# Optimization experiments

Measured on AMD Instinct MI355X. Metric: run time of the kernel, lower is better.

The kernel has to match this reference:

```python
import jax, jax.numpy as jnp
import numpy as np
from jax import lax

D = 1024      # d_model
NH = 16       # n_head
CA = 384      # adapter_channels
T = 16        # num_frames
B = 4         # videos
L = 257       # tokens = 16*16 patches + CLS
HW = 16       # spatial side


def setup_inputs() -> dict:
    key = jax.random.key(0)
    ks = jax.random.split(key, 12)
    s = 0.02
    f = lambda k, shp: jax.random.normal(k, shp, jnp.float32) * s
    return {
        'x': jax.random.normal(ks[0], (B * T, L, D), jnp.float32),
        'ln1_g': jnp.ones((D,), jnp.float32), 'ln1_b': jnp.zeros((D,), jnp.float32),
        'w_in': f(ks[1], (3 * D, D)), 'b_in': jnp.zeros((3 * D,), jnp.float32),
        'w_out': f(ks[2], (D, D)), 'b_out': jnp.zeros((D,), jnp.float32),
        'o_fc1_w': f(ks[3], (CA, D)), 'o_fc1_b': jnp.zeros((CA,), jnp.float32),
        'o_conv_w': f(ks[4], (3, 3, 1, CA)), 'o_conv_b': jnp.zeros((CA,), jnp.float32),
        'o_fc2_w': f(ks[5], (D, CA)), 'o_fc2_b': jnp.zeros((D,), jnp.float32),
        'a_fc1_w': f(ks[6], (CA, D)), 'a_fc1_b': jnp.zeros((CA,), jnp.float32),
        'a_conv_w': f(ks[7], (3, 1, CA)), 'a_conv_b': jnp.zeros((CA,), jnp.float32),
        'a_fc2_w': f(ks[8], (D, CA)), 'a_fc2_b': jnp.zeros((D,), jnp.float32),
        'ln2_g': jnp.ones((D,), jnp.float32), 'ln2_b': jnp.zeros((D,), jnp.float32),
        'mlp_fc_w': f(ks[9], (4 * D, D)), 'mlp_fc_b': jnp.zeros((4 * D,), jnp.float32),
        'mlp_proj_w': f(ks[10], (D, 4 * D)), 'mlp_proj_b': jnp.zeros((D,), jnp.float32),
    }


def _ln(x, g, b):
    # fp32 LayerNorm (matches CLIP LayerNorm subclass)
    x32 = x.astype(jnp.float32)
    mu = jnp.mean(x32, -1, keepdims=True)
    var = jnp.mean(jnp.square(x32 - mu), -1, keepdims=True)
    return ((x32 - mu) * lax.rsqrt(var + 1e-5) * g + b).astype(x.dtype)


def _mha(x, w_in, b_in, w_out, b_out):
    BT, Lq, C = x.shape
    hd = C // NH
    qkv = x @ w_in.T + b_in                       # (BT, L, 3C)
    q, k, v = jnp.split(qkv, 3, axis=-1)
    sh = lambda t: t.reshape(BT, Lq, NH, hd).transpose(0, 2, 1, 3)  # (BT, H, L, hd)
    q, k, v = sh(q), sh(k), sh(v)
    scores = jnp.einsum('bhqd,bhkd->bhqk', q * (hd ** -0.5), k)
    attn = jax.nn.softmax(scores, axis=-1)
    out = jnp.einsum('bhqk,bhkd->bhqd', attn, v)
    out = out.transpose(0, 2, 1, 3).reshape(BT, Lq, C)
    return out @ w_out.T + b_out


def _offset_adapter(x, fc1_w, fc1_b, conv_w, conv_b, fc2_w, fc2_b):
    BT, Lx, C = x.shape
    Bv = BT // T
    xs = x[:, 1:, :].reshape(Bv, T, Lx - 1, C)          # drop CLS
    former = jnp.concatenate([xs[:, :1], xs[:, :-1]], axis=1)
    off = xs - former                                    # temporal diff
    off = off @ fc1_w.T + fc1_b                          # (B, T, HW*HW, Ca)
    off = off.reshape(Bv * T, HW, HW, CA)
    # depthwise (1,3,3) Conv3d: kernel size 1 along T -> per-frame 3x3 depthwise conv
    off = lax.conv_general_dilated(off, conv_w, (1, 1), [(1, 1), (1, 1)],
                                   dimension_numbers=('NHWC', 'HWIO', 'NHWC'),
                                   feature_group_count=CA) + conv_b
    off = off.reshape(BT, Lx - 1, CA)
    return off @ fc2_w.T + fc2_b                         # (BT, L-1, C)


def _adapter2(x, a_fc1_w, a_fc1_b, a_conv_w, a_conv_b, a_fc2_w, a_fc2_b,
              o_fc1_w, o_fc1_b, o_conv_w, o_conv_b, o_fc2_w, o_fc2_b):
    BT, Lx, C = x.shape
    Bv = BT // T
    off = _offset_adapter(x, o_fc1_w, o_fc1_b, o_conv_w, o_conv_b, o_fc2_w, o_fc2_b)
    y = x @ a_fc1_w.T + a_fc1_b                          # (BT, L, Ca)
    y = y.reshape(Bv, T, Lx, CA).transpose(0, 2, 1, 3).reshape(Bv * Lx, T, CA)
    # depthwise Conv1d along the temporal axis
    y = lax.conv_general_dilated(y, a_conv_w, (1,), [(1, 1)],
                                 dimension_numbers=('NWC', 'WIO', 'NWC'),
                                 feature_group_count=CA) + a_conv_b
    y = y.reshape(Bv, Lx, T, CA).transpose(0, 2, 1, 3).reshape(BT, Lx, CA)
    y = y @ a_fc2_w.T + a_fc2_b                          # (BT, L, C)
    x_id = x.at[:, 1:, :].add(off)
    return y + x_id


def _block(x, ln1_g, ln1_b, w_in, b_in, w_out, b_out,
           a_fc1_w, a_fc1_b, a_conv_w, a_conv_b, a_fc2_w, a_fc2_b,
           o_fc1_w, o_fc1_b, o_conv_w, o_conv_b, o_fc2_w, o_fc2_b,
           ln2_g, ln2_b, mlp_fc_w, mlp_fc_b, mlp_proj_w, mlp_proj_b):
    x = x + _mha(_ln(x, ln1_g, ln1_b), w_in, b_in, w_out, b_out)
    x = _adapter2(x, a_fc1_w, a_fc1_b, a_conv_w, a_conv_b, a_fc2_w, a_fc2_b,
                  o_fc1_w, o_fc1_b, o_conv_w, o_conv_b, o_fc2_w, o_fc2_b)
    h = _ln(x, ln2_g, ln2_b) @ mlp_fc_w.T + mlp_fc_b
    h = h * jax.nn.sigmoid(1.702 * h)                    # QuickGELU
    return x + h @ mlp_proj_w.T + mlp_proj_b


def reference(x, ln1_g, ln1_b, w_in, b_in, w_out, b_out,
              o_fc1_w, o_fc1_b, o_conv_w, o_conv_b, o_fc2_w, o_fc2_b,
              a_fc1_w, a_fc1_b, a_conv_w, a_conv_b, a_fc2_w, a_fc2_b,
              ln2_g, ln2_b, mlp_fc_w, mlp_fc_b, mlp_proj_w, mlp_proj_b):
    return _block(x, ln1_g, ln1_b, w_in, b_in, w_out, b_out,
                  a_fc1_w, a_fc1_b, a_conv_w, a_conv_b, a_fc2_w, a_fc2_b,
                  o_fc1_w, o_fc1_b, o_conv_w, o_conv_b, o_fc2_w, o_fc2_b,
                  ln2_g, ln2_b, mlp_fc_w, mlp_fc_b, mlp_proj_w, mlp_proj_b)
```

## Files before the change

kernel.cpp:

```cpp
#include <hip/hip_runtime.h>
#include <cstdint>
#include <cstddef>


typedef unsigned short u16;
typedef __attribute__((ext_vector_type(4))) float  f32x4;
typedef __attribute__((ext_vector_type(8))) short  bf16x8;
typedef __attribute__((ext_vector_type(4))) unsigned int u32x4;

#define AS1 __attribute__((address_space(1)))
#define AS3 __attribute__((address_space(3)))

__device__ __forceinline__ float bf2f(u16 u) {
  unsigned int x = ((unsigned int)u) << 16;
  return __builtin_bit_cast(float, x);
}
__device__ __forceinline__ u16 f2bf(float f) {
  unsigned int x = __builtin_bit_cast(unsigned int, f);
  x = x + 0x7fffu + ((x >> 16) & 1u);
  return (u16)(x >> 16);
}
__device__ __forceinline__ unsigned int pack2(float a, float b) {
  return (unsigned int)f2bf(a) | ((unsigned int)f2bf(b) << 16);
}
__device__ __forceinline__ int imin(int a, int b) { return a < b ? a : b; }

__device__ __forceinline__ void gload_lds16(const void* g, void* l) {
  __builtin_amdgcn_global_load_lds((const AS1 unsigned int*)g,
                                   (AS3 unsigned int*)l, 16, 0, 0);
}

__global__ __launch_bounds__(256) void cvt_weights(
    const float* __restrict__ w_in, const float* __restrict__ w_out,
    const float* __restrict__ ofc1, const float* __restrict__ ofc2,
    const float* __restrict__ afc1, const float* __restrict__ afc2,
    const float* __restrict__ mfc,  const float* __restrict__ mproj,
    u16* __restrict__ dst)
{
  long i4 = (long)blockIdx.x * 256 + threadIdx.x;
  long e = i4 * 4;
  const float* src; long base;
  if      (e < 3145728L) { src = w_in;  base = 0L; }
  else if (e < 4194304L) { src = w_out; base = 3145728L; }
  else if (e < 4587520L) { src = ofc1;  base = 4194304L; }
  else if (e < 4980736L) { src = ofc2;  base = 4587520L; }
  else if (e < 5373952L) { src = afc1;  base = 4980736L; }
  else if (e < 5767168L) { src = afc2;  base = 5373952L; }
  else if (e < 9961472L) { src = mfc;   base = 5767168L; }
  else                   { src = mproj; base = 9961472L; }
  float4 v = *(const float4*)(src + (e - base));
  uint2 o; o.x = pack2(v.x, v.y); o.y = pack2(v.z, v.w);
  *(uint2*)(dst + e) = o;
}

__global__ __launch_bounds__(256) void ln_bf16(
    const float* __restrict__ x, const float* __restrict__ g,
    const float* __restrict__ b, u16* __restrict__ out)
{
  int row = blockIdx.x;
  const float4* xr = (const float4*)(x + (size_t)row * 1024);
  float4 v = xr[threadIdx.x];
  float s = v.x + v.y + v.z + v.w;
  float q = v.x * v.x + v.y * v.y + v.z * v.z + v.w * v.w;
  #pragma unroll
  for (int m = 1; m < 64; m <<= 1) { s += __shfl_xor(s, m); q += __shfl_xor(q, m); }
  __shared__ float ss[4], qq[4];
  if ((threadIdx.x & 63) == 0) { ss[threadIdx.x >> 6] = s; qq[threadIdx.x >> 6] = q; }
  __syncthreads();
  s = ss[0] + ss[1] + ss[2] + ss[3];
  q = qq[0] + qq[1] + qq[2] + qq[3];
  float mu = s * (1.f / 1024.f);
  float var = q * (1.f / 1024.f) - mu * mu;
  float rs = rsqrtf(var + 1e-5f);
  float4 gg = ((const float4*)g)[threadIdx.x];
  float4 bb = ((const float4*)b)[threadIdx.x];
  float o0 = (v.x - mu) * rs * gg.x + bb.x;
  float o1 = (v.y - mu) * rs * gg.y + bb.y;
  float o2 = (v.z - mu) * rs * gg.z + bb.z;
  float o3 = (v.w - mu) * rs * gg.w + bb.w;
  uint2 o; o.x = pack2(o0, o1); o.y = pack2(o2, o3);
  *(uint2*)(out + (size_t)row * 1024 + threadIdx.x * 4) = o;
}

__global__ __launch_bounds__(256) void diff_bf16(
    const float* __restrict__ x1, u16* __restrict__ out)
{
  int i = blockIdx.x * 256 + threadIdx.x;
  int r = i >> 8;
  int c4 = i & 255;
  int f = r >> 8;
  int p = r & 255;
  int t = f & 15;
  int rowA = f * 257 + 1 + p;
  int rowB = (t == 0) ? rowA : (f - 1) * 257 + 1 + p;
  float4 a = ((const float4*)(x1 + (size_t)rowA * 1024))[c4];
  float4 b = ((const float4*)(x1 + (size_t)rowB * 1024))[c4];
  uint2 o; o.x = pack2(a.x - b.x, a.y - b.y); o.y = pack2(a.z - b.z, a.w - b.w);
  *(uint2*)(out + (size_t)r * 1024 + c4 * 4) = o;
}

__global__ __launch_bounds__(256) void dwconv3x3(
    const u16* __restrict__ in, const float* __restrict__ w,
    const float* __restrict__ bias, u16* __restrict__ out)
{
  int idx = blockIdx.x * 256 + threadIdx.x;
  int c = idx % 384;
  int pos = idx / 384;
  int xx = pos & 15, yy = (pos >> 4) & 15, f = pos >> 8;
  float acc = bias[c];
  #pragma unroll
  for (int kh = 0; kh < 3; kh++) {
    int y2 = yy + kh - 1;
    if (y2 < 0 || y2 > 15) continue;
    #pragma unroll
    for (int kw = 0; kw < 3; kw++) {
      int x2 = xx + kw - 1;
      if (x2 < 0 || x2 > 15) continue;
      acc += bf2f(in[((size_t)(f * 256 + y2 * 16 + x2)) * 384 + c]) * w[(kh * 3 + kw) * 384 + c];
    }
  }
  out[(size_t)idx] = f2bf(acc);
}

__global__ __launch_bounds__(256) void dwconv1d(
    const u16* __restrict__ in, const float* __restrict__ w,
    const float* __restrict__ bias, u16* __restrict__ out)
{
  int idx = blockIdx.x * 256 + threadIdx.x;
  int c = idx % 384;
  int rl = idx / 384;
  int bt = rl / 257, l = rl % 257;
  int bv = bt >> 4, t = bt & 15;
  float acc = bias[c];
  #pragma unroll
  for (int dt = 0; dt < 3; dt++) {
    int tt = t + dt - 1;
    if (tt < 0 || tt > 15) continue;
    acc += bf2f(in[((size_t)((bv * 16 + tt) * 257 + l)) * 384 + c]) * w[dt * 384 + c];
  }
  out[(size_t)idx] = f2bf(acc);
}

enum { EPI_BF16 = 0, EPI_GELU = 1, EPI_RES = 2, EPI_ACC = 3, EPI_ACC_SKIPCLS = 4 };

template <int EPI>
__global__ __launch_bounds__(256) void gemm_bt(
    const u16* __restrict__ A, const u16* __restrict__ B,
    const float* __restrict__ bias,
    float* __restrict__ outF, u16* __restrict__ outB,
    const float* __restrict__ resid,
    int M, int N, int K)
{
  __shared__ u16 As[128 * 64];
  __shared__ u16 Bs[128 * 64];
  const int t = threadIdx.x, l = t & 63, w = t >> 6;
  const int row0 = blockIdx.x * 128, col0 = blockIdx.y * 128;
  const int wr = w >> 1, wc = w & 1;
  const int lo = l & 15, hi = l >> 4;
  const int larow = l >> 3, lacol = (l & 7) * 8;

  f32x4 acc[4][4];
  const f32x4 z = {0.f, 0.f, 0.f, 0.f};
  #pragma unroll
  for (int m = 0; m < 4; m++)
    #pragma unroll
    for (int n = 0; n < 4; n++) acc[m][n] = z;

  for (int k0 = 0; k0 < K; k0 += 64) {
    #pragma unroll
    for (int i = 0; i < 4; i++) {
      int rr = i * 32 + w * 8 + larow;
      int ra = row0 + rr; ra = (ra < M) ? ra : (M - 1);
      gload_lds16(A + (size_t)ra * K + k0 + lacol, As + i * 2048 + w * 512);
      gload_lds16(B + (size_t)(col0 + rr) * K + k0 + lacol, Bs + i * 2048 + w * 512);
    }
    __syncthreads();
    #pragma unroll
    for (int kk = 0; kk < 2; kk++) {
      bf16x8 af[4], bfr[4];
      #pragma unroll
      for (int m = 0; m < 4; m++)
        af[m] = __builtin_bit_cast(bf16x8,
          *(const u32x4*)&As[(wr * 64 + m * 16 + lo) * 64 + kk * 32 + hi * 8]);
      #pragma unroll
      for (int n = 0; n < 4; n++)
        bfr[n] = __builtin_bit_cast(bf16x8,
          *(const u32x4*)&Bs[(wc * 64 + n * 16 + lo) * 64 + kk * 32 + hi * 8]);
      #pragma unroll
      for (int m = 0; m < 4; m++)
        #pragma unroll
        for (int n = 0; n < 4; n++)
          acc[m][n] = __builtin_amdgcn_mfma_f32_16x16x32_bf16(af[m], bfr[n], acc[m][n], 0, 0, 0);
    }
    __syncthreads();
  }

  const int rbase = row0 + wr * 64, cbase = col0 + wc * 64;
  #pragma unroll
  for (int n = 0; n < 4; n++) {
    int colc = cbase + n * 16 + lo;
    float bv = bias[colc];
    #pragma unroll
    for (int m = 0; m < 4; m++) {
      int rr0 = rbase + m * 16 + hi * 4;
      #pragma unroll
      for (int j = 0; j < 4; j++) {
        int r = rr0 + j;
        if (r >= M) continue;
        float v = acc[m][n][j] + bv;
        if constexpr (EPI == EPI_BF16) {
          outB[(size_t)r * N + colc] = f2bf(v);
        } else if constexpr (EPI == EPI_GELU) {
          float gv = v / (1.f + __expf(-1.702f * v));
          outB[(size_t)r * N + colc] = f2bf(gv);
        } else if constexpr (EPI == EPI_RES) {
          float sres = resid[(size_t)r * N + colc] + v;
          outF[(size_t)r * N + colc] = sres;
          outB[(size_t)r * N + colc] = f2bf(sres);
        } else if constexpr (EPI == EPI_ACC) {
          outF[(size_t)r * N + colc] += v;
        } else {
          int rm = (r >> 8) * 257 + (r & 255) + 1;
          outF[(size_t)rm * N + colc] += v;
        }
      }
    }
  }
}

template <int EPI>
__global__ __launch_bounds__(512, 2) void gemm256(
    const u16* __restrict__ A, const u16* __restrict__ B,
    const float* __restrict__ bias,
    float* __restrict__ outF, u16* __restrict__ outB,
    const float* __restrict__ resid,
    int M, int N, int K, int gm)
{
  __shared__ u16 lds[49152];
  const int tid = threadIdx.x;
  const int w = tid >> 6, lane = tid & 63;
  const int lo = lane & 15, hi = lane >> 4;
  const int wm = w >> 2, wn = w & 3;

  const int nwg = gridDim.x, orig = blockIdx.x;
  const int q = nwg >> 3, r = nwg & 7;
  const int xcd = orig & 7, jj = orig >> 3;
  const int wgid = (xcd < r ? xcd * (q + 1) : r * (q + 1) + (xcd - r) * q) + jj;
  const int tm = wgid % gm, tn = wgid / gm;
  const int row0 = tm * 256, col0 = tn * 256;

  const int pr8 = tid >> 3;
  const int rb  = (((tid & 7) ^ (pr8 & 7)) << 4);
  const int sr0 = (pr8 << 1) | (rb >> 6);
  const int scol = (rb & 63) >> 1;
  const int ar0 = imin(row0 + sr0, M - 1);
  const int ar1 = imin(row0 + 128 + sr0, M - 1);
  const u16* aS0 = A + (size_t)ar0 * K + scol;
  const u16* aS1 = A + (size_t)ar1 * K + scol;
  const u16* bS0 = B + (size_t)(col0 + sr0) * K + scol;
  const u16* bS1 = B + (size_t)(col0 + 128 + sr0) * K + scol;
  u16* ldsA = lds;
  u16* ldsB = lds + 24576;
  const int wOff = w * 512;

  auto stage = [&](int b, int kt) {
    const int k0 = kt << 5;
    gload_lds16(aS0 + k0, ldsA + b * 8192 + wOff);
    gload_lds16(aS1 + k0, ldsA + b * 8192 + 4096 + wOff);
    gload_lds16(bS0 + k0, ldsB + b * 8192 + wOff);
    gload_lds16(bS1 + k0, ldsB + b * 8192 + 4096 + wOff);
  };

  const int ax = (((lo & 1) << 5) | (hi << 3)) ^ ((lo >> 1) << 3);
  const u16* aR = ldsA + (wm * 64 + (lo >> 1)) * 64 + ax;
  const u16* bR = ldsB + (wn * 32 + (lo >> 1)) * 64 + ax;

  f32x4 acc[8][4];
  const f32x4 z = {0.f, 0.f, 0.f, 0.f};
  #pragma unroll
  for (int m = 0; m < 8; m++)
    #pragma unroll
    for (int n = 0; n < 4; n++) acc[m][n] = z;

  auto compute = [&](int b) {
    const u16* ap = aR + b * 8192;
    const u16* bp = bR + b * 8192;
    bf16x8 af[8], bv[4];
    #pragma unroll
    for (int n = 0; n < 4; n++)
      bv[n] = __builtin_bit_cast(bf16x8, *(const u32x4*)(bp + n * 512));
    #pragma unroll
    for (int m = 0; m < 8; m++)
      af[m] = __builtin_bit_cast(bf16x8, *(const u32x4*)(ap + m * 512));
    #pragma unroll
    for (int m = 0; m < 8; m++)
      #pragma unroll
      for (int n = 0; n < 4; n++)
        acc[m][n] = __builtin_amdgcn_mfma_f32_16x16x32_bf16(af[m], bv[n], acc[m][n], 0, 0, 0);
  };

  const int NT = K >> 5;
  stage(0, 0);
  stage(1, 1);
  asm volatile("s_waitcnt vmcnt(4)" ::: "memory");
  __builtin_amdgcn_s_barrier();
  asm volatile("" ::: "memory");

  int bcur = 0, bnx2 = 2;
  for (int t = 0; t < NT - 2; ++t) {
    stage(bnx2, t + 2);
    compute(bcur);
    asm volatile("s_waitcnt vmcnt(4)" ::: "memory");
    __builtin_amdgcn_s_barrier();
    asm volatile("" ::: "memory");
    bcur = (bcur == 2) ? 0 : bcur + 1;
    bnx2 = (bnx2 == 2) ? 0 : bnx2 + 1;
  }
  compute(bcur);
  asm volatile("s_waitcnt vmcnt(0)" ::: "memory");
  __builtin_amdgcn_s_barrier();
  asm volatile("" ::: "memory");
  bcur = (bcur == 2) ? 0 : bcur + 1;
  compute(bcur);

  const int rbase = row0 + wm * 128, cbase = col0 + wn * 64;
  #pragma unroll
  for (int n = 0; n < 4; n++) {
    int colc = cbase + n * 16 + lo;
    float bvv = bias[colc];
    #pragma unroll
    for (int m = 0; m < 8; m++) {
      int rr0 = rbase + m * 16 + hi * 4;
      #pragma unroll
      for (int j = 0; j < 4; j++) {
        int rr = rr0 + j;
        if (rr >= M) continue;
        float v = acc[m][n][j] + bvv;
        if constexpr (EPI == EPI_BF16) {
          outB[(size_t)rr * N + colc] = f2bf(v);
        } else if constexpr (EPI == EPI_GELU) {
          float gv = v / (1.f + __expf(-1.702f * v));
          outB[(size_t)rr * N + colc] = f2bf(gv);
        } else if constexpr (EPI == EPI_RES) {
          float sres = resid[(size_t)rr * N + colc] + v;
          outF[(size_t)rr * N + colc] = sres;
          outB[(size_t)rr * N + colc] = f2bf(sres);
        } else if constexpr (EPI == EPI_ACC) {
          outF[(size_t)rr * N + colc] += v;
        } else {
          int rm = (rr >> 8) * 257 + (rr & 255) + 1;
          outF[(size_t)rm * N + colc] += v;
        }
      }
    }
  }
}

__global__ __launch_bounds__(256) void attn_kernel(
    const u16* __restrict__ qkv, u16* __restrict__ out)
{
  __shared__ u16 Vt[64 * 296];
  __shared__ u16 Ps[4][16 * 136];
  const int bt = blockIdx.x >> 4;
  const int h  = blockIdx.x & 15;
  const int t  = threadIdx.x, l = t & 63, w = t >> 6;
  const int lo = l & 15, hi = l >> 4;
  const size_t base = (size_t)bt * 257 * 3072 + (size_t)h * 64;

  for (int ch = t; ch < 257 * 8; ch += 256) {
    int r = ch >> 3, s8 = ch & 7;
    u32x4 v = *(const u32x4*)(qkv + base + (size_t)r * 3072 + 2048 + s8 * 8);
    union { u32x4 v4; u16 us[8]; } cv; cv.v4 = v;
    #pragma unroll
    for (int i = 0; i < 8; i++) Vt[(s8 * 8 + i) * 296 + r] = cv.us[i];
  }
  for (int ch = t; ch < 64 * 39; ch += 256)
    Vt[(ch / 39) * 296 + 257 + (ch % 39)] = 0;
  __syncthreads();

  for (int c = w; c < 17; c += 4) {
    int qr = c * 16 + lo; qr = (qr < 257) ? qr : 256;
    const u16* qp = qkv + base + (size_t)qr * 3072 + hi * 8;
    bf16x8 q0 = __builtin_bit_cast(bf16x8, *(const u32x4*)qp);
    bf16x8 q1 = __builtin_bit_cast(bf16x8, *(const u32x4*)(qp + 32));

    f32x4 s[17];
    #pragma unroll
    for (int tt = 0; tt < 17; tt++) {
      int kr = tt * 16 + lo; kr = (kr < 257) ? kr : 256;
      const u16* kp = qkv + base + (size_t)kr * 3072 + 1024 + hi * 8;
      bf16x8 k0 = __builtin_bit_cast(bf16x8, *(const u32x4*)kp);
      bf16x8 k1 = __builtin_bit_cast(bf16x8, *(const u32x4*)(kp + 32));
      f32x4 a = {0.f, 0.f, 0.f, 0.f};
      a = __builtin_amdgcn_mfma_f32_16x16x32_bf16(q0, k0, a, 0, 0, 0);
      a = __builtin_amdgcn_mfma_f32_16x16x32_bf16(q1, k1, a, 0, 0, 0);
      s[tt] = a;
    }
    float mx[4] = {-1e30f, -1e30f, -1e30f, -1e30f};
    #pragma unroll
    for (int tt = 0; tt < 17; tt++) {
      int key = tt * 16 + lo;
      #pragma unroll
      for (int j = 0; j < 4; j++) {
        float v = s[tt][j] * 0.125f;
        v = (key < 257) ? v : -1e30f;
        s[tt][j] = v;
        mx[j] = fmaxf(mx[j], v);
      }
    }
    #pragma unroll
    for (int j = 0; j < 4; j++)
      #pragma unroll
      for (int msk = 1; msk < 16; msk <<= 1) mx[j] = fmaxf(mx[j], __shfl_xor(mx[j], msk));
    float sm[4] = {0.f, 0.f, 0.f, 0.f};
    #pragma unroll
    for (int tt = 0; tt < 17; tt++)
      #pragma unroll
      for (int j = 0; j < 4; j++) {
        float p = __expf(s[tt][j] - mx[j]);
        s[tt][j] = p; sm[j] += p;
      }
    #pragma unroll
    for (int j = 0; j < 4; j++) {
      #pragma unroll
      for (int msk = 1; msk < 16; msk <<= 1) sm[j] += __shfl_xor(sm[j], msk);
      sm[j] = 1.f / sm[j];
    }

    u16* P = &Ps[w][0];
    f32x4 o[4];
    #pragma unroll
    for (int n = 0; n < 4; n++) o[n] = (f32x4){0.f, 0.f, 0.f, 0.f};
    #pragma unroll
    for (int ph = 0; ph < 3; ph++) {
      const int TT = (ph < 2) ? 8 : 1;
      #pragma unroll
      for (int ti = 0; ti < TT; ti++) {
        int tt = ph * 8 + ti;
        #pragma unroll
        for (int j = 0; j < 4; j++)
          P[(hi * 4 + j) * 136 + ti * 16 + lo] = f2bf(s[tt][j] * sm[j]);
      }
      if (ph == 2) {
        #pragma unroll
        for (int j = 0; j < 4; j++) P[(hi * 4 + j) * 136 + 16 + lo] = 0;
      }
      const int NKS = (ph < 2) ? 4 : 1;
      #pragma unroll
      for (int ks = 0; ks < NKS; ks++) {
        bf16x8 af = __builtin_bit_cast(bf16x8,
          *(const u32x4*)&P[lo * 136 + ks * 32 + hi * 8]);
        #pragma unroll
        for (int n = 0; n < 4; n++) {
          bf16x8 bfr = __builtin_bit_cast(bf16x8,
            *(const u32x4*)&Vt[(n * 16 + lo) * 296 + ph * 128 + ks * 32 + hi * 8]);
          o[n] = __builtin_amdgcn_mfma_f32_16x16x32_bf16(af, bfr, o[n], 0, 0, 0);
        }
      }
    }
    #pragma unroll
    for (int n = 0; n < 4; n++)
      #pragma unroll
      for (int j = 0; j < 4; j++) {
        int row = c * 16 + hi * 4 + j;
        if (row < 257)
          out[(size_t)(bt * 257 + row) * 1024 + h * 64 + n * 16 + lo] = f2bf(o[n][j]);
      }
  }
}

extern "C" void kernel_launch(void* const* d_in, const int* in_sizes, int n_in,
                              void* d_out, int out_size, void* d_ws, size_t ws_size,
                              hipStream_t stream)
{
  const float* x       = (const float*)d_in[0];
  const float* ln1_g   = (const float*)d_in[1];
  const float* ln1_b   = (const float*)d_in[2];
  const float* w_in    = (const float*)d_in[3];
  const float* b_in    = (const float*)d_in[4];
  const float* w_out   = (const float*)d_in[5];
  const float* b_out   = (const float*)d_in[6];
  const float* o_fc1_w = (const float*)d_in[7];
  const float* o_fc1_b = (const float*)d_in[8];
  const float* o_conv_w= (const float*)d_in[9];
  const float* o_conv_b= (const float*)d_in[10];
  const float* o_fc2_w = (const float*)d_in[11];
  const float* o_fc2_b = (const float*)d_in[12];
  const float* a_fc1_w = (const float*)d_in[13];
  const float* a_fc1_b = (const float*)d_in[14];
  const float* a_conv_w= (const float*)d_in[15];
  const float* a_conv_b= (const float*)d_in[16];
  const float* a_fc2_w = (const float*)d_in[17];
  const float* a_fc2_b = (const float*)d_in[18];
  const float* ln2_g   = (const float*)d_in[19];
  const float* ln2_b   = (const float*)d_in[20];
  const float* mfc_w   = (const float*)d_in[21];
  const float* mfc_b   = (const float*)d_in[22];
  const float* mproj_w = (const float*)d_in[23];
  const float* mproj_b = (const float*)d_in[24];
  float* xo = (float*)d_out;

  char* ws = (char*)d_ws;
  u16* WB = (u16*)ws;
  u16* R0 = (u16*)(ws + 28311552);
  u16* R1 = (u16*)(ws + 28311552 + 33685504);
  u16* R2 = (u16*)(ws + 28311552 + 33685504 + 101056512);
  u16* w_in_bf  = WB + 0;
  u16* w_out_bf = WB + 3145728;
  u16* ofc1_bf  = WB + 4194304;
  u16* ofc2_bf  = WB + 4587520;
  u16* afc1_bf  = WB + 4980736;
  u16* afc2_bf  = WB + 5373952;
  u16* mfc_bf   = WB + 5767168;
  u16* mproj_bf = WB + 9961472;
  u16* off1 = R1;
  u16* offc = R1 + 6291456;
  u16* y1   = R1 + 12582912;
  u16* yc   = R1 + 12582912 + 6316032;

  cvt_weights<<<13824, 256, 0, stream>>>(w_in, w_out, o_fc1_w, o_fc2_w,
                                         a_fc1_w, a_fc2_w, mfc_w, mproj_w, WB);
  ln_bf16<<<16448, 256, 0, stream>>>(x, ln1_g, ln1_b, R0);
  gemm256<EPI_BF16><<<65 * 12, 512, 0, stream>>>(
      R0, w_in_bf, b_in, nullptr, R1, nullptr, 16448, 3072, 1024, 65);
  attn_kernel<<<1024, 256, 0, stream>>>(R1, R2);
  gemm256<EPI_RES><<<65 * 4, 512, 0, stream>>>(
      R2, w_out_bf, b_out, xo, R0, x, 16448, 1024, 1024, 65);
  diff_bf16<<<16384, 256, 0, stream>>>(xo, R2);
  gemm_bt<EPI_BF16><<<dim3(128, 3), 256, 0, stream>>>(
      R2, ofc1_bf, o_fc1_b, nullptr, off1, nullptr, 16384, 384, 1024);
  dwconv3x3<<<24576, 256, 0, stream>>>(off1, o_conv_w, o_conv_b, offc);
  gemm256<EPI_ACC_SKIPCLS><<<64 * 4, 512, 0, stream>>>(
      offc, ofc2_bf, o_fc2_b, xo, nullptr, nullptr, 16384, 1024, 384, 64);
  gemm_bt<EPI_BF16><<<dim3(129, 3), 256, 0, stream>>>(
      R0, afc1_bf, a_fc1_b, nullptr, y1, nullptr, 16448, 384, 1024);
  dwconv1d<<<24672, 256, 0, stream>>>(y1, a_conv_w, a_conv_b, yc);
  gemm256<EPI_ACC><<<65 * 4, 512, 0, stream>>>(
      yc, afc2_bf, a_fc2_b, xo, nullptr, nullptr, 16448, 1024, 384, 65);
  ln_bf16<<<16448, 256, 0, stream>>>(xo, ln2_g, ln2_b, R0);
  gemm256<EPI_GELU><<<65 * 16, 512, 0, stream>>>(
      R0, mfc_bf, mfc_b, nullptr, R1, nullptr, 16448, 4096, 1024, 65);
  gemm256<EPI_ACC><<<65 * 4, 512, 0, stream>>>(
      R1, mproj_bf, mproj_b, xo, nullptr, nullptr, 16448, 1024, 4096, 65);
}
```

Baseline: 1.483 ms.

## Restructure 256x256 GEMM mainloop into double-buffered K=64 ping-pong schedule

Replaces the triple-buffered K=32 pipeline with a double-buffered K=64 tile whose mainloop is split into four MFMA quadrants, with LDS fragment loads and global prefetch interleaved between barriers and raised wave priority around the MFMA blocks. It also changes the tile-to-workgroup mapping to group four N-tiles per super-group for better L2 reuse, and uses a new XOR swizzle for LDS reads. This aims to hide LDS and global latency behind matrix ops, at the cost of more barriers per iteration and larger LDS use (128KB), which could affect occupancy under launch_bounds(512,2).

```diff
diff --git a/kernel.cpp b/kernel.cpp
--- a/kernel.cpp
+++ b/kernel.cpp
@@ -236,7 +236,7 @@
     const float* __restrict__ resid,
     int M, int N, int K, int gm)
 {
-  __shared__ u16 lds[49152];
+  __shared__ u16 lds[65536];
   const int tid = threadIdx.x;
   const int w = tid >> 6, lane = tid & 63;
   const int lo = lane & 15, hi = lane >> 4;
@@ -245,35 +245,36 @@
   const int nwg = gridDim.x, orig = blockIdx.x;
   const int q = nwg >> 3, r = nwg & 7;
   const int xcd = orig & 7, jj = orig >> 3;
-  const int wgid = (xcd < r ? xcd * (q + 1) : r * (q + 1) + (xcd - r) * q) + jj;
-  const int tm = wgid % gm, tn = wgid / gm;
+  const int lid = (xcd < r ? xcd * (q + 1) : r * (q + 1) + (xcd - r) * q) + jj;
+  const int sg = lid / (gm * 4), rem = lid - sg * (gm * 4);
+  const int tm = rem >> 2, tn = sg * 4 + (rem & 3);
   const int row0 = tm * 256, col0 = tn * 256;
 
-  const int pr8 = tid >> 3;
-  const int rb  = (((tid & 7) ^ (pr8 & 7)) << 4);
-  const int sr0 = (pr8 << 1) | (rb >> 6);
-  const int scol = (rb & 63) >> 1;
-  const int ar0 = imin(row0 + sr0, M - 1);
-  const int ar1 = imin(row0 + 128 + sr0, M - 1);
-  const u16* aS0 = A + (size_t)ar0 * K + scol;
-  const u16* aS1 = A + (size_t)ar1 * K + scol;
-  const u16* bS0 = B + (size_t)(col0 + sr0) * K + scol;
-  const u16* bS1 = B + (size_t)(col0 + 128 + sr0) * K + scol;
-  u16* ldsA = lds;
-  u16* ldsB = lds + 24576;
-  const int wOff = w * 512;
-
-  auto stage = [&](int b, int kt) {
-    const int k0 = kt << 5;
-    gload_lds16(aS0 + k0, ldsA + b * 8192 + wOff);
-    gload_lds16(aS1 + k0, ldsA + b * 8192 + 4096 + wOff);
-    gload_lds16(bS0 + k0, ldsB + b * 8192 + wOff);
-    gload_lds16(bS1 + k0, ldsB + b * 8192 + 4096 + wOff);
+  const int srow = w * 8 + (lane >> 3);
+  const int scolEl = ((lane & 7) ^ (lane >> 3)) << 3;
+  const u16* aS[4]; const u16* bS[4];
+  #pragma unroll
+  for (int i = 0; i < 4; i++) {
+    int ar = imin(row0 + i * 64 + srow, M - 1);
+    aS[i] = A + (size_t)ar * K + scolEl;
+    bS[i] = B + (size_t)(col0 + i * 64 + srow) * K + scolEl;
+  }
+  auto stageA = [&](int c2, int kOff) {
+    u16* d = (u16*)lds + c2 * 32768 + (w << 9);
+    #pragma unroll
+    for (int i = 0; i < 4; i++) gload_lds16(aS[i] + kOff, d + i * 4096);
   };
-
-  const int ax = (((lo & 1) << 5) | (hi << 3)) ^ ((lo >> 1) << 3);
-  const u16* aR = ldsA + (wm * 64 + (lo >> 1)) * 64 + ax;
-  const u16* bR = ldsB + (wn * 32 + (lo >> 1)) * 64 + ax;
+  auto stageB = [&](int c2, int kOff) {
+    u16* d = (u16*)lds + c2 * 32768 + 16384 + (w << 9);
+    #pragma unroll
+    for (int i = 0; i < 4; i++) gload_lds16(bS[i] + kOff, d + i * 4096);
+  };
+
+  const int swz = (lo & 7) << 3;
+  const int cK0 = (hi << 3) ^ swz;
+  const int cK1 = ((hi << 3) | 32) ^ swz;
+  const int aRowE = (wm * 128 + lo) * 64;
+  const int bRowE = (wn * 64 + lo) * 64;
 
   f32x4 acc[8][4];
   const f32x4 z = {0.f, 0.f, 0.f, 0.f};
@@ -282,46 +283,82 @@
     #pragma unroll
     for (int n = 0; n < 4; n++) acc[m][n] = z;
 
-  auto compute = [&](int b) {
-    const u16* ap = aR + b * 8192;
-    const u16* bp = bR + b * 8192;
-    bf16x8 af[8], bv[4];
-    #pragma unroll
-    for (int n = 0; n < 4; n++)
-      bv[n] = __builtin_bit_cast(bf16x8, *(const u32x4*)(bp + n * 512));
-    #pragma unroll
-    for (int m = 0; m < 8; m++)
-      af[m] = __builtin_bit_cast(bf16x8, *(const u32x4*)(ap + m * 512));
-    #pragma unroll
-    for (int m = 0; m < 8; m++)
-      #pragma unroll
-      for (int n = 0; n < 4; n++)
-        acc[m][n] = __builtin_amdgcn_mfma_f32_16x16x32_bf16(af[m], bv[n], acc[m][n], 0, 0, 0);
-  };
-
-  const int NT = K >> 5;
-  stage(0, 0);
-  stage(1, 1);
-  asm volatile("s_waitcnt vmcnt(4)" ::: "memory");
-  __builtin_amdgcn_s_barrier();
-  asm volatile("" ::: "memory");
-
-  int bcur = 0, bnx2 = 2;
-  for (int t = 0; t < NT - 2; ++t) {
-    stage(bnx2, t + 2);
-    compute(bcur);
-    asm volatile("s_waitcnt vmcnt(4)" ::: "memory");
-    __builtin_amdgcn_s_barrier();
-    asm volatile("" ::: "memory");
-    bcur = (bcur == 2) ? 0 : bcur + 1;
-    bnx2 = (bnx2 == 2) ? 0 : bnx2 + 1;
-  }
-  compute(bcur);
+  bf16x8 aF[4][2], bF0[2][2], bF1[2][2];
+
+#define LOADA(BA, MH)                                                          \
+  { _Pragma("unroll")                                                          \
+    for (int mi = 0; mi < 4; mi++) {                                           \
+      const u16* p = (BA) + aRowE + ((MH) * 4 + mi) * 1024;                    \
+      aF[mi][0] = __builtin_bit_cast(bf16x8, *(const u32x4*)(p + cK0));        \
+      aF[mi][1] = __builtin_bit_cast(bf16x8, *(const u32x4*)(p + cK1));        \
+    } }
+#define LOADB(BB, BF, NH)                                                      \
+  { _Pragma("unroll")                                                          \
+    for (int ni = 0; ni < 2; ni++) {                                           \
+      const u16* p = (BB) + bRowE + ((NH) * 2 + ni) * 1024;                    \
+      BF[ni][0] = __builtin_bit_cast(bf16x8, *(const u32x4*)(p + cK0));        \
+      BF[ni][1] = __builtin_bit_cast(bf16x8, *(const u32x4*)(p + cK1));        \
+    } }
+#define MFMA16(MH, NH, BF)                                                     \
+  { _Pragma("unroll")                                                          \
+    for (int mi = 0; mi < 4; mi++)                                             \
+      _Pragma("unroll")                                                        \
+      for (int ni = 0; ni < 2; ni++)                                           \
+        _Pragma("unroll")                                                      \
+        for (int kk = 0; kk < 2; kk++)                                         \
+          acc[(MH)*4+mi][(NH)*2+ni] = __builtin_amdgcn_mfma_f32_16x16x32_bf16( \
+              aF[mi][kk], BF[ni][kk], acc[(MH)*4+mi][(NH)*2+ni], 0, 0, 0); }
+
+  const int NT = K >> 6;
+  stageA(0, 0);
+  stageB(0, 0);
   asm volatile("s_waitcnt vmcnt(0)" ::: "memory");
   __builtin_amdgcn_s_barrier();
-  asm volatile("" ::: "memory");
-  bcur = (bcur == 2) ? 0 : bcur + 1;
-  compute(bcur);
+
+  for (int t = 0; t < NT; ++t) {
+    const int c = t & 1;
+    const u16* bufA = (const u16*)lds + c * 32768;
+    const u16* bufB = bufA + 16384;
+    const bool pf = (t + 1) < NT;
+    const int kn = (t + 1) << 6;
+
+    LOADA(bufA, 0);
+    LOADB(bufB, bF0, 0);
+    if (pf) stageA(c ^ 1, kn);
+    __builtin_amdgcn_sched_barrier(0);
+    __builtin_amdgcn_s_barrier();
+    __builtin_amdgcn_s_setprio(1);
+    MFMA16(0, 0, bF0);
+    __builtin_amdgcn_s_setprio(0);
+    __builtin_amdgcn_sched_barrier(0);
+    __builtin_amdgcn_s_barrier();
+    LOADB(bufB, bF1, 1);
+    if (pf) stageB(c ^ 1, kn);
+    __builtin_amdgcn_sched_barrier(0);
+    __builtin_amdgcn_s_barrier();
+    __builtin_amdgcn_s_setprio(1);
+    MFMA16(0, 1, bF1);
+    __builtin_amdgcn_s_setprio(0);
+    __builtin_amdgcn_sched_barrier(0);
+    __builtin_amdgcn_s_barrier();
+    LOADA(bufA, 1);
+    __builtin_amdgcn_sched_barrier(0);
+    __builtin_amdgcn_s_barrier();
+    __builtin_amdgcn_s_setprio(1);
+    MFMA16(1, 1, bF1);
+    __builtin_amdgcn_s_setprio(0);
+    __builtin_amdgcn_sched_barrier(0);
+    __builtin_amdgcn_s_barrier();
+    __builtin_amdgcn_s_setprio(1);
+    MFMA16(1, 0, bF0);
+    __builtin_amdgcn_s_setprio(0);
+    __builtin_amdgcn_sched_barrier(0);
+    asm volatile("s_waitcnt vmcnt(0)" ::: "memory");
+    __builtin_amdgcn_s_barrier();
+  }
+#undef LOADA
+#undef LOADB
+#undef MFMA16
 
   const int rbase = row0 + wm * 128, cbase = col0 + wn * 64;
   #pragma unroll
```

After: 1.473 ms. No clear change (-0.7%).
